# Kernel tuning notes

Hardware: AMD Instinct MI355X
Metric: run time of the kernel (lower is better)

Reference implementation:

```python
import jax, jax.numpy as jnp
import numpy as np
from jax import lax

EPS = 1e-12  # F.normalize eps


def _l2norm(x, axis):
    n = jnp.sqrt(jnp.sum(x * x, axis=axis, keepdims=True))
    return x / jnp.maximum(n, EPS)


def setup_inputs() -> dict:
    key = jax.random.key(0)
    k1, k2 = jax.random.split(key)
    b, t, c, E = 4, 4096, 2048, 64
    return {
        "hidden_states": jax.random.normal(k1, (b, t, c), dtype=jnp.float32),
        "sim_matrix": jax.random.normal(k2, (c, E), dtype=jnp.float32),
        "gates": jnp.zeros((E,), dtype=jnp.float32),
        "fallback_k": 2,
    }


def reference(hidden_states, sim_matrix, gates, fallback_k):
    b, t, c = hidden_states.shape
    x = hidden_states.reshape(b * t, c)
    # normalized similarity logits: cosine(x, expert) - gate
    logits = jnp.matmul(_l2norm(x, -1), _l2norm(sim_matrix, 0)) - gates  # [N, E]
    gated = jax.nn.relu(logits)
    # STE: forward is hard {0,1}, backward is identity
    hard = (gated > 0).astype(gated.dtype)
    ste_mask = gated + lax.stop_gradient(hard - gated)
    inactive = jnp.sum(hard, axis=1) == 0  # [N] rows with no active expert
    # fallback: top-k of raw logits, computed for all rows (static shape), applied only to inactive rows
    _, top_idx = lax.top_k(logits, fallback_k)  # [N, k]
    n = logits.shape[0]
    fallback_mask = jnp.zeros_like(logits).at[jnp.arange(n)[:, None], top_idx].set(1.0)
    activation_mask = jnp.where(inactive[:, None], lax.stop_gradient(fallback_mask), ste_mask)
    masked = jnp.where(activation_mask > 0, gated, -jnp.inf)
    routing_weights = jax.nn.softmax(masked, axis=-1)
    return routing_weights, logits, activation_mask
```

## Files before the change

kernel.cpp:

```cpp
#include <hip/hip_runtime.h>
#include <hip/hip_bf16.h>
#include <math.h>

#define C_DIM 2048
#define E_DIM 64
#define KC 32
#define NCHUNK (C_DIM / KC)
#define KC_BLK 12

typedef __attribute__((address_space(3))) float lds_f;
typedef const __attribute__((address_space(1))) float glb_f;

__device__ __forceinline__ float np_pairwise_2048(const float* __restrict__ a,
                                                  int stride, int lane) {
  const int g = lane >> 3, k = lane & 7;
  float half_tot[2];
#pragma unroll
  for (int h = 0; h < 2; ++h) {
    const int c0 = h * 1024 + g * 128 + k;
    float v = a[(size_t)c0 * stride];
    float r = __fmul_rn(v, v);
#pragma unroll
    for (int i = 1; i < 16; ++i) {
      v = a[(size_t)(c0 + 8 * i) * stride];
      r = __fadd_rn(r, __fmul_rn(v, v));
    }
    r = __fadd_rn(r, __shfl_xor(r, 1));
    r = __fadd_rn(r, __shfl_xor(r, 2));
    r = __fadd_rn(r, __shfl_xor(r, 4));
    r = __fadd_rn(r, __shfl_xor(r, 8));
    r = __fadd_rn(r, __shfl_xor(r, 16));
    r = __fadd_rn(r, __shfl_xor(r, 32));
    half_tot[h] = r;
  }
  return __fadd_rn(half_tot[0], half_tot[1]);
}

__global__ __launch_bounds__(256) void xnorm_kernel(const float* __restrict__ X,
                                                    float* __restrict__ den, int N) {
  const int row = blockIdx.x * 4 + (threadIdx.x >> 6);
  const int l = threadIdx.x & 63;
  if (row >= N) return;
  const float tot = np_pairwise_2048(X + (size_t)row * C_DIM, 1, l);
  if (l == 0) den[row] = fmaxf(sqrtf(tot), 1e-12f);
}

__global__ __launch_bounds__(64) void simnorm_kernel(const float* __restrict__ sim,
                                                     float* __restrict__ sT) {
  const int e = blockIdx.x;
  const int l = threadIdx.x;
  const float tot = np_pairwise_2048(sim + e, E_DIM, l);
  const float den = fmaxf(sqrtf(tot), 1e-12f);
  for (int c = l; c < C_DIM; c += 64)
    sT[(size_t)e * C_DIM + c] = sim[(size_t)c * E_DIM + e] / den;
}

__global__ __launch_bounds__(256) void gating_main(const float* __restrict__ X,
                                                   const float* __restrict__ denx,
                                                   const float* __restrict__ sT,
                                                   const float* __restrict__ gates,
                                                   const int* __restrict__ fbk,
                                                   float* __restrict__ out, int N) {
  __shared__ float smem[8192];
  const int t = threadIdx.x;
  const int w = t >> 6, l = t & 63;
  const int wr = w >> 1, we = w & 1;
  const int rg = l >> 3, eg = l & 7;
  const size_t rowbase = (size_t)blockIdx.x * 64;
  const float* Xb = X + rowbase * C_DIM;

  const int u0 = t, u1 = t + 256;
  const int r0 = u0 >> 3, cb0 = (u0 & 7) ^ ((r0 >> 2) & 7);
  const int r1 = u1 >> 3, cb1 = (u1 & 7) ^ ((r1 >> 2) & 7);
  const float d0 = denx[rowbase + r0];
  const float d1 = denx[rowbase + r1];

  float4 xr0, xr1;
  auto issueX = [&](int c0) {
    xr0 = *(const float4*)(Xb + (size_t)r0 * C_DIM + c0 + cb0 * 4);
    xr1 = *(const float4*)(Xb + (size_t)r1 * C_DIM + c0 + cb1 * 4);
  };
  auto issueS = [&](int buf, int c0) {
    glb_f* g0 = (glb_f*)(sT + (size_t)r0 * C_DIM + c0 + cb0 * 4);
    lds_f* s0 = (lds_f*)&smem[buf * 4096 + 2048 + u0 * 4];
    __builtin_amdgcn_global_load_lds((const __attribute__((address_space(1))) void*)g0,
                                     (__attribute__((address_space(3))) void*)s0, 16, 0, 0);
    glb_f* g1 = (glb_f*)(sT + (size_t)r1 * C_DIM + c0 + cb1 * 4);
    lds_f* s1 = (lds_f*)&smem[buf * 4096 + 2048 + u1 * 4];
    __builtin_amdgcn_global_load_lds((const __attribute__((address_space(1))) void*)g1,
                                     (__attribute__((address_space(3))) void*)s1, 16, 0, 0);
  };
  auto writeX = [&](int buf) {
    float4 a, b;
    a.x = xr0.x / d0; a.y = xr0.y / d0; a.z = xr0.z / d0; a.w = xr0.w / d0;
    b.x = xr1.x / d1; b.y = xr1.y / d1; b.z = xr1.z / d1; b.w = xr1.w / d1;
    *(float4*)&smem[buf * 4096 + u0 * 4] = a;
    *(float4*)&smem[buf * 4096 + u1 * 4] = b;
  };

  float ab[4][4], tt[4][4];
#pragma unroll
  for (int i = 0; i < 4; ++i)
#pragma unroll
    for (int j = 0; j < 4; ++j) ab[i][j] = 0.f;

  issueX(0);
  issueS(0, 0);
  writeX(0);
  asm volatile("s_waitcnt vmcnt(0) lgkmcnt(0)" ::: "memory");
  __builtin_amdgcn_s_barrier();
  asm volatile("" ::: "memory");

  for (int ch = 0; ch < NCHUNK; ++ch) {
    const int buf = ch & 1;
    if (ch + 1 < NCHUNK) {
      issueX((ch + 1) * KC);
      issueS(buf ^ 1, (ch + 1) * KC);
    }
    if (ch && (ch % KC_BLK) == 0) {
#pragma unroll
      for (int i = 0; i < 4; ++i)
#pragma unroll
        for (int j = 0; j < 4; ++j) {
          if (ch == KC_BLK) tt[i][j] = ab[i][j];
          else tt[i][j] = __fadd_rn(tt[i][j], ab[i][j]);
          ab[i][j] = 0.f;
        }
    }

    const int xb = buf * 4096;
    const int sb = xb + 2048;
#pragma unroll
    for (int u = 0; u < 8; ++u) {
      float4 xv[4], sv[4];
#pragma unroll
      for (int i = 0; i < 4; ++i) {
        const int row = wr * 32 + rg * 4 + i;
        xv[i] = *(const float4*)&smem[xb + row * 32 + (u ^ rg) * 4];
      }
#pragma unroll
      for (int j = 0; j < 4; ++j) {
        const int er = we * 32 + eg * 4 + j;
        sv[j] = *(const float4*)&smem[sb + er * 32 + (u ^ eg) * 4];
      }
#pragma unroll
      for (int i = 0; i < 4; ++i)
#pragma unroll
        for (int j = 0; j < 4; ++j) {
          float a = ab[i][j];
          a = fmaf(xv[i].x, sv[j].x, a);
          a = fmaf(xv[i].y, sv[j].y, a);
          a = fmaf(xv[i].z, sv[j].z, a);
          a = fmaf(xv[i].w, sv[j].w, a);
          ab[i][j] = a;
        }
    }
    asm volatile("" ::: "memory");
    if (ch + 1 < NCHUNK) writeX(buf ^ 1);
    asm volatile("s_waitcnt vmcnt(0) lgkmcnt(0)" ::: "memory");
    __builtin_amdgcn_s_barrier();
    asm volatile("" ::: "memory");
  }
#pragma unroll
  for (int i = 0; i < 4; ++i)
#pragma unroll
    for (int j = 0; j < 4; ++j) tt[i][j] = __fadd_rn(tt[i][j], ab[i][j]);

  float* lg = smem;
#pragma unroll
  for (int i = 0; i < 4; ++i) {
    const int row = wr * 32 + rg * 4 + i;
#pragma unroll
    for (int j = 0; j < 4; ++j) lg[row * 66 + we * 32 + eg * 4 + j] = tt[i][j];
  }
  __syncthreads();

  const int k = fbk[0];
  const float gate = gates[l];
  const size_t NE = (size_t)N * E_DIM;

  for (int rr = 0; rr < 16; ++rr) {
    const int row = w * 16 + rr;
    const float logit = __fadd_rn(lg[row * 66 + l], -gate);
    const float gated = fmaxf(logit, 0.f);
    const bool act = logit > 0.f;
    const unsigned long long bal = __ballot(act);
    const bool inactive = (bal == 0ull);

    float cur = logit;
    bool fb = false;
    for (int tk = 0; tk < k; ++tk) {
      float v = cur;
      int idx = l;
#pragma unroll
      for (int off = 32; off >= 1; off >>= 1) {
        const float ov = __shfl_xor(v, off);
        const int oi = __shfl_xor(idx, off);
        if (ov > v || (ov == v && oi < idx)) { v = ov; idx = oi; }
      }
      if (l == idx) { cur = -INFINITY; fb = true; }
    }

    const float mask = inactive ? (fb ? 1.f : 0.f) : (act ? 1.f : 0.f);
    const float masked = (mask > 0.f) ? gated : -INFINITY;
    float m = masked;
#pragma unroll
    for (int off = 32; off >= 1; off >>= 1) m = fmaxf(m, __shfl_xor(m, off));
    const float p = (mask > 0.f) ? expf(masked - m) : 0.f;
    float s = p;
#pragma unroll
    for (int off = 32; off >= 1; off >>= 1) s += __shfl_xor(s, off);
    const float wgt = p / s;

    const size_t gr = rowbase + row;
    out[gr * E_DIM + l] = wgt;
    out[NE + gr * E_DIM + l] = logit;
    out[2 * NE + gr * E_DIM + l] = mask;
  }
}

extern "C" void kernel_launch(void* const* d_in, const int* in_sizes, int n_in,
                              void* d_out, int out_size, void* d_ws, size_t ws_size,
                              hipStream_t stream) {
  (void)n_in; (void)out_size; (void)ws_size;
  const float* X = (const float*)d_in[0];
  const float* sim = (const float*)d_in[1];
  const float* gates = (const float*)d_in[2];
  const int* fbk = (const int*)d_in[3];
  float* out = (float*)d_out;
  float* den = (float*)d_ws;
  float* sT = (float*)d_ws + 16384;
  const int N = in_sizes[0] / C_DIM;

  hipLaunchKernelGGL(xnorm_kernel, dim3(N / 4), dim3(256), 0, stream, X, den, N);
  hipLaunchKernelGGL(simnorm_kernel, dim3(E_DIM), dim3(64), 0, stream, sim, sT);
  hipLaunchKernelGGL(gating_main, dim3(N / 64), dim3(256), 0, stream, X, den, sT, gates, fbk, out, N);
}
```

Measured before the change: 361.3 us.

## Rework norm kernels and read normalized sim directly from global in gating GEMM

Result: slower. 735.5 us (+103.6%).

```diff
diff --git a/kernel.cpp b/kernel.cpp
--- a/kernel.cpp
+++ b/kernel.cpp
@@ -4,63 +4,87 @@
 
 #define C_DIM 2048
 #define E_DIM 64
-#define KC 32
-#define NCHUNK (C_DIM / KC)
-#define KC_BLK 12
-
-typedef __attribute__((address_space(3))) float lds_f;
-typedef const __attribute__((address_space(1))) float glb_f;
-
-__device__ __forceinline__ float np_pairwise_2048(const float* __restrict__ a,
-                                                  int stride, int lane) {
-  const int g = lane >> 3, k = lane & 7;
-  float half_tot[2];
-#pragma unroll
-  for (int h = 0; h < 2; ++h) {
-    const int c0 = h * 1024 + g * 128 + k;
-    float v = a[(size_t)c0 * stride];
-    float r = __fmul_rn(v, v);
-#pragma unroll
-    for (int i = 1; i < 16; ++i) {
-      v = a[(size_t)(c0 + 8 * i) * stride];
-      r = __fadd_rn(r, __fmul_rn(v, v));
-    }
-    r = __fadd_rn(r, __shfl_xor(r, 1));
-    r = __fadd_rn(r, __shfl_xor(r, 2));
-    r = __fadd_rn(r, __shfl_xor(r, 4));
-    r = __fadd_rn(r, __shfl_xor(r, 8));
-    r = __fadd_rn(r, __shfl_xor(r, 16));
-    r = __fadd_rn(r, __shfl_xor(r, 32));
-    half_tot[h] = r;
-  }
-  return __fadd_rn(half_tot[0], half_tot[1]);
-}
+#define KC 64
+#define NCHUNK 32
+#define FOLD_EVERY 6
+
 
 __global__ __launch_bounds__(256) void xnorm_kernel(const float* __restrict__ X,
                                                     float* __restrict__ den, int N) {
-  const int row = blockIdx.x * 4 + (threadIdx.x >> 6);
-  const int l = threadIdx.x & 63;
-  if (row >= N) return;
-  const float tot = np_pairwise_2048(X + (size_t)row * C_DIM, 1, l);
-  if (l == 0) den[row] = fmaxf(sqrtf(tot), 1e-12f);
-}
-
-__global__ __launch_bounds__(64) void simnorm_kernel(const float* __restrict__ sim,
-                                                     float* __restrict__ sT) {
-  const int e = blockIdx.x;
-  const int l = threadIdx.x;
-  const float tot = np_pairwise_2048(sim + e, E_DIM, l);
+  const int w = threadIdx.x >> 6, l = threadIdx.x & 63;
+  const int row = blockIdx.x * 8 + w * 2 + (l >> 5);
+  const int task = l & 31;
+  const int b = task >> 1, a = (task & 1) * 4;
+  const float* p0 = X + (size_t)row * C_DIM + b * 128 + a;
+
+  float4 v = *(const float4*)p0;
+  float ax = __fmul_rn(v.x, v.x), ay = __fmul_rn(v.y, v.y);
+  float az = __fmul_rn(v.z, v.z), aw = __fmul_rn(v.w, v.w);
+#pragma unroll
+  for (int p = 1; p < 16; ++p) {
+    v = *(const float4*)(p0 + p * 8);
+    ax = __fadd_rn(ax, __fmul_rn(v.x, v.x));
+    ay = __fadd_rn(ay, __fmul_rn(v.y, v.y));
+    az = __fadd_rn(az, __fmul_rn(v.z, v.z));
+    aw = __fadd_rn(aw, __fmul_rn(v.w, v.w));
+  }
+  float r = __fadd_rn(__fadd_rn(ax, ay), __fadd_rn(az, aw));
+  r = __fadd_rn(r, __shfl_xor(r, 1));
+  r = __fadd_rn(r, __shfl_xor(r, 2));
+  r = __fadd_rn(r, __shfl_xor(r, 4));
+  r = __fadd_rn(r, __shfl_xor(r, 8));
+  r = __fadd_rn(r, __shfl_xor(r, 16));
+  if (task == 0 && row < N) den[row] = fmaxf(sqrtf(r), 1e-12f);
+}
+
+__global__ __launch_bounds__(64) void simnorm_a_kernel(const float* __restrict__ sim,
+                                                       float* __restrict__ Bsum) {
+  const int b = blockIdx.x, l = threadIdx.x;
+  const float* base = sim + (size_t)(b * 128) * E_DIM + l;
+#define SQ(c) __fmul_rn(base[(c) * E_DIM], base[(c) * E_DIM])
+  float a0 = SQ(0), a1 = SQ(1), a2 = SQ(2), a3 = SQ(3);
+  float a4 = SQ(4), a5 = SQ(5), a6 = SQ(6), a7 = SQ(7);
+#pragma unroll
+  for (int g = 1; g < 16; ++g) {
+    a0 = __fadd_rn(a0, SQ(g * 8 + 0)); a1 = __fadd_rn(a1, SQ(g * 8 + 1));
+    a2 = __fadd_rn(a2, SQ(g * 8 + 2)); a3 = __fadd_rn(a3, SQ(g * 8 + 3));
+    a4 = __fadd_rn(a4, SQ(g * 8 + 4)); a5 = __fadd_rn(a5, SQ(g * 8 + 5));
+    a6 = __fadd_rn(a6, SQ(g * 8 + 6)); a7 = __fadd_rn(a7, SQ(g * 8 + 7));
+  }
+#undef SQ
+  const float left = __fadd_rn(__fadd_rn(a0, a1), __fadd_rn(a2, a3));
+  const float right = __fadd_rn(__fadd_rn(a4, a5), __fadd_rn(a6, a7));
+  Bsum[b * E_DIM + l] = __fadd_rn(left, right);
+}
+
+__global__ __launch_bounds__(256) void simnorm_b_kernel(const float* __restrict__ sim,
+                                                        const float* __restrict__ Bsum,
+                                                        float* __restrict__ sT) {
+  const int e = blockIdx.x, t = threadIdx.x;
+  float B[16];
+#pragma unroll
+  for (int b = 0; b < 16; ++b) B[b] = Bsum[b * E_DIM + e];
+  float c01 = __fadd_rn(B[0], B[1]), c23 = __fadd_rn(B[2], B[3]);
+  float c45 = __fadd_rn(B[4], B[5]), c67 = __fadd_rn(B[6], B[7]);
+  float c89 = __fadd_rn(B[8], B[9]), cab = __fadd_rn(B[10], B[11]);
+  float ccd = __fadd_rn(B[12], B[13]), cef = __fadd_rn(B[14], B[15]);
+  float q0 = __fadd_rn(c01, c23), q1 = __fadd_rn(c45, c67);
+  float q2 = __fadd_rn(c89, cab), q3 = __fadd_rn(ccd, cef);
+  const float tot = __fadd_rn(__fadd_rn(q0, q1), __fadd_rn(q2, q3));
   const float den = fmaxf(sqrtf(tot), 1e-12f);
-  for (int c = l; c < C_DIM; c += 64)
+#pragma unroll
+  for (int i = 0; i < 8; ++i) {
+    const int c = t + i * 256;
     sT[(size_t)e * C_DIM + c] = sim[(size_t)c * E_DIM + e] / den;
-}
-
-__global__ __launch_bounds__(256) void gating_main(const float* __restrict__ X,
-                                                   const float* __restrict__ denx,
-                                                   const float* __restrict__ sT,
-                                                   const float* __restrict__ gates,
-                                                   const int* __restrict__ fbk,
-                                                   float* __restrict__ out, int N) {
+  }
+}
+
+__global__ __launch_bounds__(256, 1) void gating_main(const float* __restrict__ X,
+                                                      const float* __restrict__ denx,
+                                                      const float* __restrict__ sT,
+                                                      const float* __restrict__ gates,
+                                                      const int* __restrict__ fbk,
+                                                      float* __restrict__ out, int N) {
   __shared__ float smem[8192];
   const int t = threadIdx.x;
   const int w = t >> 6, l = t & 63;
@@ -69,33 +93,31 @@
   const size_t rowbase = (size_t)blockIdx.x * 64;
   const float* Xb = X + rowbase * C_DIM;
 
-  const int u0 = t, u1 = t + 256;
-  const int r0 = u0 >> 3, cb0 = (u0 & 7) ^ ((r0 >> 2) & 7);
-  const int r1 = u1 >> 3, cb1 = (u1 & 7) ^ ((r1 >> 2) & 7);
-  const float d0 = denx[rowbase + r0];
-  const float d1 = denx[rowbase + r1];
-
-  float4 xr0, xr1;
-  auto issueX = [&](int c0) {
-    xr0 = *(const float4*)(Xb + (size_t)r0 * C_DIM + c0 + cb0 * 4);
-    xr1 = *(const float4*)(Xb + (size_t)r1 * C_DIM + c0 + cb1 * 4);
-  };
-  auto issueS = [&](int buf, int c0) {
-    glb_f* g0 = (glb_f*)(sT + (size_t)r0 * C_DIM + c0 + cb0 * 4);
-    lds_f* s0 = (lds_f*)&smem[buf * 4096 + 2048 + u0 * 4];
-    __builtin_amdgcn_global_load_lds((const __attribute__((address_space(1))) void*)g0,
-                                     (__attribute__((address_space(3))) void*)s0, 16, 0, 0);
-    glb_f* g1 = (glb_f*)(sT + (size_t)r1 * C_DIM + c0 + cb1 * 4);
-    lds_f* s1 = (lds_f*)&smem[buf * 4096 + 2048 + u1 * 4];
-    __builtin_amdgcn_global_load_lds((const __attribute__((address_space(1))) void*)g1,
-                                     (__attribute__((address_space(3))) void*)s1, 16, 0, 0);
+  int skidx[4];
+  float sden[4];
+  const float* sgsrc[4];
+#pragma unroll
+  for (int it = 0; it < 4; ++it) {
+    const int u = t + 256 * it;
+    const int srow = u >> 4, sphys = u & 15;
+    skidx[it] = sphys ^ ((srow >> 2) & 15);
+    sden[it] = denx[rowbase + srow];
+    sgsrc[it] = Xb + (size_t)srow * C_DIM + skidx[it] * 4;
+  }
+
+  float4 xr[4];
+  auto loadX = [&](int ch) {
+#pragma unroll
+    for (int it = 0; it < 4; ++it) xr[it] = *(const float4*)(sgsrc[it] + ch * KC);
   };
   auto writeX = [&](int buf) {
-    float4 a, b;
-    a.x = xr0.x / d0; a.y = xr0.y / d0; a.z = xr0.z / d0; a.w = xr0.w / d0;
-    b.x = xr1.x / d1; b.y = xr1.y / d1; b.z = xr1.z / d1; b.w = xr1.w / d1;
-    *(float4*)&smem[buf * 4096 + u0 * 4] = a;
-    *(float4*)&smem[buf * 4096 + u1 * 4] = b;
+#pragma unroll
+    for (int it = 0; it < 4; ++it) {
+      float4 o;
+      o.x = xr[it].x / sden[it]; o.y = xr[it].y / sden[it];
+      o.z = xr[it].z / sden[it]; o.w = xr[it].w / sden[it];
+      *(float4*)&smem[buf * 4096 + (t + 256 * it) * 4] = o;
+    }
   };
 
   float ab[4][4], tt[4][4];
@@ -104,45 +126,40 @@
 #pragma unroll
     for (int j = 0; j < 4; ++j) ab[i][j] = 0.f;
 
-  issueX(0);
-  issueS(0, 0);
+  const int swz = (wr * 8 + rg) & 15;
+  const float* sTj[4];
+#pragma unroll
+  for (int j = 0; j < 4; ++j) sTj[j] = sT + (size_t)(we * 32 + eg * 4 + j) * C_DIM;
+
+  loadX(0);
   writeX(0);
-  asm volatile("s_waitcnt vmcnt(0) lgkmcnt(0)" ::: "memory");
-  __builtin_amdgcn_s_barrier();
-  asm volatile("" ::: "memory");
+  __syncthreads();
 
   for (int ch = 0; ch < NCHUNK; ++ch) {
-    const int buf = ch & 1;
-    if (ch + 1 < NCHUNK) {
-      issueX((ch + 1) * KC);
-      issueS(buf ^ 1, (ch + 1) * KC);
-    }
-    if (ch && (ch % KC_BLK) == 0) {
+    if (ch && (ch % FOLD_EVERY) == 0) {
 #pragma unroll
       for (int i = 0; i < 4; ++i)
 #pragma unroll
         for (int j = 0; j < 4; ++j) {
-          if (ch == KC_BLK) tt[i][j] = ab[i][j];
+          if (ch == FOLD_EVERY) tt[i][j] = ab[i][j];
           else tt[i][j] = __fadd_rn(tt[i][j], ab[i][j]);
           ab[i][j] = 0.f;
         }
     }
-
-    const int xb = buf * 4096;
-    const int sb = xb + 2048;
-#pragma unroll
-    for (int u = 0; u < 8; ++u) {
+    const int buf = ch & 1;
+    if (ch + 1 < NCHUNK) loadX(ch + 1);
+    const int xbase = buf * 4096;
+#pragma unroll
+    for (int u = 0; u < 16; ++u) {
       float4 xv[4], sv[4];
 #pragma unroll
       for (int i = 0; i < 4; ++i) {
         const int row = wr * 32 + rg * 4 + i;
-        xv[i] = *(const float4*)&smem[xb + row * 32 + (u ^ rg) * 4];
+        xv[i] = *(const float4*)&smem[xbase + row * 64 + ((u ^ swz) * 4)];
       }
 #pragma unroll
-      for (int j = 0; j < 4; ++j) {
-        const int er = we * 32 + eg * 4 + j;
-        sv[j] = *(const float4*)&smem[sb + er * 32 + (u ^ eg) * 4];
-      }
+      for (int j = 0; j < 4; ++j)
+        sv[j] = *(const float4*)(sTj[j] + ch * KC + u * 4);
 #pragma unroll
       for (int i = 0; i < 4; ++i)
 #pragma unroll
@@ -155,11 +172,8 @@
           ab[i][j] = a;
         }
     }
-    asm volatile("" ::: "memory");
     if (ch + 1 < NCHUNK) writeX(buf ^ 1);
-    asm volatile("s_waitcnt vmcnt(0) lgkmcnt(0)" ::: "memory");
-    __builtin_amdgcn_s_barrier();
-    asm volatile("" ::: "memory");
+    __syncthreads();
   }
 #pragma unroll
   for (int i = 0; i < 4; ++i)
@@ -190,13 +204,13 @@
     float cur = logit;
     bool fb = false;
     for (int tk = 0; tk < k; ++tk) {
-      float v = cur;
+      float v2 = cur;
       int idx = l;
 #pragma unroll
       for (int off = 32; off >= 1; off >>= 1) {
-        const float ov = __shfl_xor(v, off);
+        const float ov = __shfl_xor(v2, off);
         const int oi = __shfl_xor(idx, off);
-        if (ov > v || (ov == v && oi < idx)) { v = ov; idx = oi; }
+        if (ov > v2 || (ov == v2 && oi < idx)) { v2 = ov; idx = oi; }
       }
       if (l == idx) { cur = -INFINITY; fb = true; }
     }
@@ -230,9 +244,11 @@
   float* out = (float*)d_out;
   float* den = (float*)d_ws;
   float* sT = (float*)d_ws + 16384;
+  float* Bsum = (float*)d_ws + 16384 + 131072;
   const int N = in_sizes[0] / C_DIM;
 
-  hipLaunchKernelGGL(xnorm_kernel, dim3(N / 4), dim3(256), 0, stream, X, den, N);
-  hipLaunchKernelGGL(simnorm_kernel, dim3(E_DIM), dim3(64), 0, stream, sim, sT);
+  hipLaunchKernelGGL(xnorm_kernel, dim3(N / 8), dim3(256), 0, stream, X, den, N);
+  hipLaunchKernelGGL(simnorm_a_kernel, dim3(16), dim3(64), 0, stream, sim, Bsum);
+  hipLaunchKernelGGL(simnorm_b_kernel, dim3(E_DIM), dim3(256), 0, stream, sim, Bsum, sT);
   hipLaunchKernelGGL(gating_main, dim3(N / 64), dim3(256), 0, stream, X, den, sT, gates, fbk, out, N);
 }
```
